# Optimization experiments

Measured on AMD Instinct MI355X. Metric: run time of the kernel, lower is better.

## Reference

```python
import jax, jax.numpy as jnp
import numpy as np

EPS = 1e-5
H_DIM = 64  # hidden_dim


def _bn_relu(x, gamma, beta):
    # torch BatchNorm1d in train mode on [B, C, N]: stats per-channel over (B, N).
    # x here is [B, N, C] (we skip the permutes; math is identical).
    mean = jnp.mean(x, axis=(0, 1))
    var = jnp.var(x, axis=(0, 1))  # biased, matches torch normalization
    return jax.nn.relu((x - mean) * jax.lax.rsqrt(var + EPS) * gamma + beta)


def _make_G(inc):
    # G = DV^{-1/2} H W invDE H^T DV^{-1/2} with W = I, expressed as
    # elementwise diagonal scaling instead of dense diag matmuls.
    H = jax.lax.stop_gradient(inc)  # built under torch.no_grad
    dv = jnp.sum(H, axis=1)  # node degrees [n]
    de = jnp.sum(H, axis=0)  # hyperedge degrees [e]
    Hn = H * (dv ** -0.5)[:, None]          # DV2 @ H
    return (Hn * (1.0 / de)[None, :]) @ Hn.T  # [n, n]


def _gconv_cat(G, node_vec, hidden_flat, W, b, gamma, beta):
    # SHGConv_concate.forward
    B, N, _ = node_vec.shape
    h = hidden_flat.reshape(B, N, H_DIM)
    x = jnp.concatenate([node_vec, h], axis=-1) @ W  # [B, N, out]
    g = jnp.einsum('nm,bmd->bnd', G, x)
    out = _bn_relu(g, gamma, beta) + x + b
    return out.reshape(B, -1)


def _outlayer(G, x0, x1, W0, W1, b, gamma, beta):
    # SHGConv.forward (hidden_dim -> 2)
    h0 = x0 @ W0
    h1 = x1 @ W1
    o0 = _bn_relu(jnp.einsum('nm,bmd->bnd', G, h0), gamma, beta) + h0
    o1 = _bn_relu(jnp.einsum('nm,bmd->bnd', G, h1), gamma, beta) + h1
    return (o0 + o1) / 2.0 + b


def _cell(G, x_t, h, p):
    # STHGCell: GRU-style gating; note torch chunks the FLATTENED [B, N*2H]
    # tensor along dim 1, which we replicate exactly.
    B, N, _ = x_t.shape
    NH = N * H_DIM
    conc = jax.nn.sigmoid(_gconv_cat(G, x_t, h, p['W1'], p['b1'], p['g1'], p['e1']))
    r, u = conc[:, :NH], conc[:, NH:]
    c = jnp.tanh(_gconv_cat(G, x_t, r * h, p['W2'], p['b2'], p['g2'], p['e2']))
    return u * h + (1.0 - u) * c


def setup_inputs() -> dict:
    key = jax.random.key(0)
    ks = jax.random.split(key, 16)
    N, E, D, B, S = 512, 128, 16, 32, 32
    # sparse binary incidence with every node/edge covered (positive degrees)
    Hm = (jax.random.uniform(ks[0], (N, E)) < 0.05).astype(jnp.float32)
    Hm = Hm.at[jnp.arange(N), jnp.arange(N) % E].set(1.0)
    s = 0.1
    return {
        'inputs': jax.random.normal(ks[1], (B, S, N, D), jnp.float32),
        'inc': Hm,
        'gc1_W': jax.random.normal(ks[2], (D + H_DIM, 2 * H_DIM)) * s,
        'gc1_b': jax.random.normal(ks[3], (2 * H_DIM,)) * s,
        'gc1_gamma': jnp.ones((2 * H_DIM,)) + 0.1 * jax.random.normal(ks[4], (2 * H_DIM,)),
        'gc1_beta': jax.random.normal(ks[5], (2 * H_DIM,)) * s,
        'gc2_W': jax.random.normal(ks[6], (D + H_DIM, H_DIM)) * s,
        'gc2_b': jax.random.normal(ks[7], (H_DIM,)) * s,
        'gc2_gamma': jnp.ones((H_DIM,)) + 0.1 * jax.random.normal(ks[8], (H_DIM,)),
        'gc2_beta': jax.random.normal(ks[9], (H_DIM,)) * s,
        'out_W0': jax.random.normal(ks[10], (H_DIM, 2)) * s,
        'out_W1': jax.random.normal(ks[11], (H_DIM, 2)) * s,
        'out_b': jax.random.normal(ks[12], (2,)) * s,
        'out_gamma': jnp.ones((2,)) + 0.1 * jax.random.normal(ks[13], (2,)),
        'out_beta': jax.random.normal(ks[14], (2,)) * s,
    }


def reference(inputs, inc, gc1_W, gc1_b, gc1_gamma, gc1_beta,
              gc2_W, gc2_b, gc2_gamma, gc2_beta,
              out_W0, out_W1, out_b, out_gamma, out_beta):
    B, S, N, D = inputs.shape
    G = _make_G(inc)
    p = dict(W1=gc1_W, b1=gc1_b, g1=gc1_gamma, e1=gc1_beta,
             W2=gc2_W, b2=gc2_b, g2=gc2_gamma, e2=gc2_beta)
    x_tm = jnp.transpose(inputs, (1, 0, 2, 3))  # [S, B, N, D]
    h0 = jnp.zeros((B, N * H_DIM), inputs.dtype)

    def bwd_step(h, xt):
        hn = _cell(G, xt, h, p)
        return hn, hn.reshape(B, N, H_DIM)

    _, feats_b = jax.lax.scan(bwd_step, h0, x_tm[::-1])
    feats1 = feats_b[::-1]  # time order; feats1[t] pairs with forward step t

    def fwd_step(h, xf):
        xt, f1 = xf
        hn = _cell(G, xt, h, p)
        o0 = hn.reshape(B, N, H_DIM)
        pred = _outlayer(G, o0, f1, out_W0, out_W1, out_b, out_gamma, out_beta)
        return hn, (pred, o0)

    _, (preds, feats0) = jax.lax.scan(fwd_step, h0, (x_tm, feats1))
    # 'pred': [B, S, N, 2], 'feat': stacked feats0 [B, S, N, H]
    return jnp.transpose(preds, (1, 0, 2, 3)), jnp.transpose(feats0, (1, 0, 2, 3))
```

## Files before the change

### kernel.cpp

```cpp
#include <hip/hip_runtime.h>
#include <math.h>

#define B_   32
#define S_   32
#define N_   512
#define D_   16
#define H_   64
#define EPS_ 1e-5f
#define CNT_ 16384.0f
#define SNH_ 1048576
#define NH_  32768
#define LDST 72

typedef __attribute__((ext_vector_type(8))) short short8v;
typedef __attribute__((ext_vector_type(8))) _Float16 f16x8;
typedef __attribute__((ext_vector_type(4))) float f32x4;

__device__ __forceinline__ float sigm(float x) { return 1.0f / (1.0f + __expf(-x)); }

__device__ __forceinline__ unsigned short f2h(float x) {
  union { _Float16 h; unsigned short u; } c;
  c.h = (_Float16)x;
  return c.u;
}
__device__ __forceinline__ float h2f(unsigned short u) {
  union { _Float16 h; unsigned short u; } c;
  c.u = u;
  return (float)c.h;
}

__global__ __launch_bounds__(256) void k_deg(const float* __restrict__ Hm,
                                             float* __restrict__ Hs,
                                             float* __restrict__ Hd) {
  __shared__ float sdv[512];
  __shared__ float sde[128];
  __shared__ float tmp[256];
  const int tid = threadIdx.x;
  const int e = tid & 127, half = tid >> 7;
  float p = 0.f;
  for (int r = 0; r < 256; ++r) p += Hm[(half * 256 + r) * 128 + e];
  tmp[tid] = p;
  for (int n = tid; n < 512; n += 256) {
    float s = 0.f;
    for (int k = 0; k < 128; k += 4) {
      float4 v = *(const float4*)&Hm[n * 128 + k];
      s += v.x + v.y + v.z + v.w;
    }
    sdv[n] = s;
  }
  __syncthreads();
  if (tid < 128) sde[tid] = tmp[tid] + tmp[tid + 128];
  __syncthreads();
  for (int i = tid; i < 512 * 128; i += 256) {
    int n = i >> 7, ee = i & 127;
    float hv = Hm[i];
    float hs = hv * rsqrtf(sdv[n]);
    Hs[i] = hs;
    Hd[i] = hs / sde[ee];
  }
}

__global__ __launch_bounds__(256) void g_build(const float* __restrict__ A,
                                               const float* __restrict__ B,
                                               float* __restrict__ C) {
  constexpr int KT = 16;
  __shared__ float As[KT][64];
  __shared__ float Bs[KT][64];
  const int tid = threadIdx.x;
  const int tx = tid & 15, ty = tid >> 4;
  const int n0 = blockIdx.x * 64, m0 = blockIdx.y * 64;
  float acc[4][4];
#pragma unroll
  for (int i = 0; i < 4; ++i)
#pragma unroll
    for (int j = 0; j < 4; ++j) acc[i][j] = 0.f;
  const int ra = tid >> 2, ca = (tid & 3) * 4;
  for (int k0 = 0; k0 < 128; k0 += KT) {
    {
      float4 v = *(const float4*)&A[(size_t)(m0 + ra) * 128 + k0 + ca];
      As[ca + 0][ra] = v.x; As[ca + 1][ra] = v.y;
      As[ca + 2][ra] = v.z; As[ca + 3][ra] = v.w;
    }
    {
      float4 v = *(const float4*)&B[(size_t)(n0 + ra) * 128 + k0 + ca];
      Bs[ca + 0][ra] = v.x; Bs[ca + 1][ra] = v.y;
      Bs[ca + 2][ra] = v.z; Bs[ca + 3][ra] = v.w;
    }
    __syncthreads();
#pragma unroll
    for (int kk = 0; kk < KT; ++kk) {
      float a[4], bv[4];
#pragma unroll
      for (int i = 0; i < 4; ++i) a[i] = As[kk][ty * 4 + i];
#pragma unroll
      for (int j = 0; j < 4; ++j) bv[j] = Bs[kk][tx * 4 + j];
#pragma unroll
      for (int i = 0; i < 4; ++i)
#pragma unroll
        for (int j = 0; j < 4; ++j) acc[i][j] = fmaf(a[i], bv[j], acc[i][j]);
    }
    __syncthreads();
  }
#pragma unroll
  for (int i = 0; i < 4; ++i)
#pragma unroll
    for (int j = 0; j < 4; ++j)
      C[(size_t)(m0 + ty * 4 + i) * 512 + n0 + tx * 4 + j] = acc[i][j];
}

__global__ __launch_bounds__(256) void g2h(const float* __restrict__ G,
                                           unsigned short* __restrict__ Gh) {
  int i = (blockIdx.x * 256 + threadIdx.x) * 4;
  float4 v = *(const float4*)&G[i];
  ushort4 o;
  o.x = f2h(v.x); o.y = f2h(v.y); o.z = f2h(v.z); o.w = f2h(v.w);
  *(ushort4*)&Gh[i] = o;
}

__global__ __launch_bounds__(256) void gmfma(
    const unsigned short* __restrict__ A, const unsigned short* __restrict__ Bf,
    float* __restrict__ C, int Nt, float* __restrict__ stats,
    int chmask, int dirColblks, int dirBase, int sqOff) {
  __shared__ __align__(16) unsigned short As[128 * LDST];
  __shared__ __align__(16) unsigned short Bs[64 * LDST];
  const int tid = threadIdx.x;
  const int lane = tid & 63;
  const int w = tid >> 6, wr = w >> 1, wc = w & 1;
  const int l15 = lane & 15, l4 = lane >> 4;
  const int col0 = blockIdx.x * 64, n0 = blockIdx.y * 128;
  const int srow = tid >> 3, sch = (tid & 7) * 8;

  f32x4 acc[4][2];
#pragma unroll
  for (int mi = 0; mi < 4; ++mi)
#pragma unroll
    for (int ni = 0; ni < 2; ++ni) acc[mi][ni] = (f32x4)0.f;

  short8v pa[4], pb[2];
#pragma unroll
  for (int q = 0; q < 4; ++q)
    pa[q] = *(const short8v*)&A[(size_t)(n0 + srow + q * 32) * 512 + sch];
#pragma unroll
  for (int q = 0; q < 2; ++q)
    pb[q] = *(const short8v*)&Bf[(size_t)(col0 + srow + q * 32) * 512 + sch];

  for (int k0 = 0; k0 < 512; k0 += 64) {
#pragma unroll
    for (int q = 0; q < 4; ++q)
      *(short8v*)&As[(srow + q * 32) * LDST + sch] = pa[q];
#pragma unroll
    for (int q = 0; q < 2; ++q)
      *(short8v*)&Bs[(srow + q * 32) * LDST + sch] = pb[q];
    __syncthreads();
    if (k0 < 448) {
      int kn = k0 + 64;
#pragma unroll
      for (int q = 0; q < 4; ++q)
        pa[q] = *(const short8v*)&A[(size_t)(n0 + srow + q * 32) * 512 + kn + sch];
#pragma unroll
      for (int q = 0; q < 2; ++q)
        pb[q] = *(const short8v*)&Bf[(size_t)(col0 + srow + q * 32) * 512 + kn + sch];
    }
#pragma unroll
    for (int kk = 0; kk < 64; kk += 32) {
      f16x8 av[4], bv[2];
#pragma unroll
      for (int mi = 0; mi < 4; ++mi)
        av[mi] = *(const f16x8*)&As[(wr * 64 + mi * 16 + l15) * LDST + kk + l4 * 8];
#pragma unroll
      for (int ni = 0; ni < 2; ++ni)
        bv[ni] = *(const f16x8*)&Bs[(wc * 32 + ni * 16 + l15) * LDST + kk + l4 * 8];
#pragma unroll
      for (int mi = 0; mi < 4; ++mi)
#pragma unroll
        for (int ni = 0; ni < 2; ++ni)
          acc[mi][ni] = __builtin_amdgcn_mfma_f32_16x16x32_f16(av[mi], bv[ni],
                                                               acc[mi][ni], 0, 0, 0);
    }
    __syncthreads();
  }

  float cs[2] = {0.f, 0.f}, cq[2] = {0.f, 0.f};
#pragma unroll
  for (int mi = 0; mi < 4; ++mi)
#pragma unroll
    for (int ni = 0; ni < 2; ++ni)
#pragma unroll
      for (int r = 0; r < 4; ++r) {
        float val = acc[mi][ni][r];
        C[(size_t)(n0 + wr * 64 + mi * 16 + l4 * 4 + r) * Nt + col0 + wc * 32 + ni * 16 + l15] = val;
        cs[ni] += val;
        cq[ni] = fmaf(val, val, cq[ni]);
      }
  float* red = (float*)As;
  const int owner = wr * 4 + l4;
#pragma unroll
  for (int ni = 0; ni < 2; ++ni) {
    int cb = wc * 32 + ni * 16 + l15;
    red[cb * 8 + owner] = cs[ni];
    red[512 + cb * 8 + owner] = cq[ni];
  }
  __syncthreads();
  if (tid < 64) {
    float s = 0.f, q = 0.f;
    for (int o = 0; o < 8; ++o) { s += red[tid * 8 + o]; q += red[512 + tid * 8 + o]; }
    int base = (blockIdx.x >= dirColblks) ? dirBase : 0;
    int ch = (col0 + tid) & chmask;
    atomicAdd(&stats[base + ch], s);
    atomicAdd(&stats[base + sqOff + ch], q);
  }
}

__global__ __launch_bounds__(512) void prek(
    const float* __restrict__ inp, const float* __restrict__ W1,
    unsigned short* __restrict__ Xf1A, float* __restrict__ h,
    float* __restrict__ st1a, float* __restrict__ stoAll) {
  __shared__ float As[64 * 16];
  __shared__ float Ws[16 * 128];
  const int tid = threadIdx.x, bid = blockIdx.x;
  const int dirb = bid >> 3, m0 = (bid & 7) * 64;
  const int b = dirb & 31;
  const int t0 = (dirb < 32) ? 0 : (S_ - 1);
  float4 z; z.x = 0.f; z.y = 0.f; z.z = 0.f; z.w = 0.f;
  *(float4*)&h[(size_t)dirb * 32768 + m0 * 64 + tid * 8] = z;
  *(float4*)&h[(size_t)dirb * 32768 + m0 * 64 + tid * 8 + 4] = z;
  if (bid == 0) st1a[tid] = 0.f;
  if (bid == 1 && tid < 256) stoAll[tid] = 0.f;
  *(float4*)&Ws[tid * 4] = *(const float4*)&W1[tid * 4];
  {
    int row = tid >> 3, j = tid & 7;
    float2 iv = *(const float2*)&inp[(size_t)((b * S_ + t0) * N_ + m0 + row) * D_ + j * 2];
    As[row * 16 + j * 2] = iv.x;
    As[row * 16 + j * 2 + 1] = iv.y;
  }
  __syncthreads();
  const int tx = tid & 31, ty = tid >> 5;
  float acc[4][4];
#pragma unroll
  for (int i = 0; i < 4; ++i)
#pragma unroll
    for (int j = 0; j < 4; ++j) acc[i][j] = 0.f;
  for (int k = 0; k < 16; ++k) {
    float av[4];
#pragma unroll
    for (int i = 0; i < 4; ++i) av[i] = As[(ty * 4 + i) * 16 + k];
    float4 bv = *(const float4*)&Ws[k * 128 + tx * 4];
    float bva[4] = {bv.x, bv.y, bv.z, bv.w};
#pragma unroll
    for (int i = 0; i < 4; ++i)
#pragma unroll
      for (int j = 0; j < 4; ++j) acc[i][j] = fmaf(av[i], bva[j], acc[i][j]);
  }
#pragma unroll
  for (int j = 0; j < 4; ++j) {
    int g = dirb * 128 + tx * 4 + j;
    ushort4 o;
    o.x = f2h(acc[0][j]); o.y = f2h(acc[1][j]);
    o.z = f2h(acc[2][j]); o.w = f2h(acc[3][j]);
    *(ushort4*)&Xf1A[(size_t)g * 512 + m0 + ty * 4] = o;
  }
}

__global__ __launch_bounds__(512) void cat2k(
    const float* __restrict__ inp, const float* __restrict__ h,
    const float* __restrict__ W2, unsigned short* __restrict__ Xf2,
    const float* __restrict__ G1t, const unsigned short* __restrict__ Xf1C,
    const float* __restrict__ st1c, const float* __restrict__ g1,
    const float* __restrict__ e1, const float* __restrict__ b1,
    float* __restrict__ st2, int tf, int tb) {
  __shared__ float As[80 * 64];
  __shared__ float Ws[80 * 64];
  __shared__ float sm[128], sa[128], sb[128], sbb[128];
  const int tid = threadIdx.x, bid = blockIdx.x;
  const int dirb = bid >> 3, m0 = (bid & 7) * 64;
  const int b = dirb & 31;
  const int dir = (dirb >= 32);
  const int t = dir ? tb : tf;
  if (bid == 0 && tid < 256) st2[tid] = 0.f;
  const float* stp = st1c + (dir ? 256 : 0);
  if (tid < 128) {
    float mean = stp[tid] * (1.f / CNT_);
    float var = fmaf(stp[128 + tid], 1.f / CNT_, -mean * mean);
    float inv = rsqrtf(var + EPS_);
    sm[tid] = mean; sa[tid] = inv * g1[tid];
    sb[tid] = e1[tid]; sbb[tid] = b1[tid];
  }
  for (int i = tid * 4; i < 5120; i += 2048)
    *(float4*)&Ws[i] = *(const float4*)&W2[i];
  __syncthreads();
  const int row = tid >> 3, j = tid & 7;
  const int m = m0 + row;
  if (j < 4) {
    float4 iv = *(const float4*)&inp[(size_t)((b * S_ + t) * N_ + m) * D_ + j * 4];
    As[(j * 4 + 0) * 64 + row] = iv.x; As[(j * 4 + 1) * 64 + row] = iv.y;
    As[(j * 4 + 2) * 64 + row] = iv.z; As[(j * 4 + 3) * 64 + row] = iv.w;
  }
  {
    const int c0 = j * 8;
    const int n = m >> 1;
    const int dd = ((m & 1) << 6) + c0;
    float hva[8], gva[8];
    const float* ph = &h[(size_t)dirb * 32768 + m * 64 + c0];
    const float* pg = &G1t[(size_t)n * 8192 + dirb * 128 + dd];
    *(float4*)&hva[0] = *(const float4*)&ph[0];
    *(float4*)&hva[4] = *(const float4*)&ph[4];
    *(float4*)&gva[0] = *(const float4*)&pg[0];
    *(float4*)&gva[4] = *(const float4*)&pg[4];
#pragma unroll
    for (int i = 0; i < 8; ++i) {
      int d2 = dd + i;
      float x1v = h2f(Xf1C[(size_t)(dirb * 128 + d2) * 512 + n]);
      float pre = fmaf(gva[i] - sm[d2], sa[d2], sb[d2]);
      pre = fmaxf(pre, 0.f) + x1v + sbb[d2];
      As[(16 + c0 + i) * 64 + row] = sigm(pre) * hva[i];
    }
  }
  __syncthreads();
  const int tx = tid & 15, ty = tid >> 4;
  float acc[2][4];
#pragma unroll
  for (int i = 0; i < 2; ++i)
#pragma unroll
    for (int jj = 0; jj < 4; ++jj) acc[i][jj] = 0.f;
  for (int k = 0; k < 80; ++k) {
    float a0 = As[k * 64 + ty * 2], a1 = As[k * 64 + ty * 2 + 1];
    float4 bv = *(const float4*)&Ws[k * 64 + tx * 4];
    float bva[4] = {bv.x, bv.y, bv.z, bv.w};
#pragma unroll
    for (int jj = 0; jj < 4; ++jj) {
      acc[0][jj] = fmaf(a0, bva[jj], acc[0][jj]);
      acc[1][jj] = fmaf(a1, bva[jj], acc[1][jj]);
    }
  }
#pragma unroll
  for (int jj = 0; jj < 4; ++jj) {
    int g = dirb * 64 + tx * 4 + jj;
    ushort2 o;
    o.x = f2h(acc[0][jj]); o.y = f2h(acc[1][jj]);
    *(ushort2*)&Xf2[(size_t)g * 512 + m0 + ty * 2] = o;
  }
}

__global__ __launch_bounds__(512) void eltk(
    const float* __restrict__ inp, const float* __restrict__ G1t,
    const unsigned short* __restrict__ Xf1C, const float* __restrict__ st1c,
    const float* __restrict__ g1, const float* __restrict__ e1,
    const float* __restrict__ b1, const float* __restrict__ G2t,
    const unsigned short* __restrict__ Xf2, const float* __restrict__ st2,
    const float* __restrict__ g2, const float* __restrict__ e2,
    const float* __restrict__ b2, float* __restrict__ h,
    float* __restrict__ out1, const float* __restrict__ W1,
    unsigned short* __restrict__ Xf1N, const float* __restrict__ W0o,
    const float* __restrict__ W1o, unsigned short* __restrict__ Xo16,
    int tf, int tb, int doX1, float* __restrict__ stn) {
  __shared__ float As[64 * 80];
  __shared__ float Ws[80 * 128];
  __shared__ float sW0[128], sW1[128];
  const int tid = threadIdx.x, bid = blockIdx.x;
  const int dirb = bid >> 3, m0 = (bid & 7) * 64;
  const int b = dirb & 31;
  const int dir = (dirb >= 32);
  const int t = dir ? tb : tf;
  const int nextT = dir ? (tb - 1) : (tf + 1);
  if (bid == 0) stn[tid] = 0.f;
  if (tid < 128) { sW0[tid] = W0o[tid]; sW1[tid] = W1o[tid]; }
  __syncthreads();

  const int row = tid >> 3, co = (tid & 7) * 8;
  const int m = m0 + row;
  const int mh = m >> 1;
  const int du0 = ((m & 1) << 6) + co;
  const float* stp = st1c + (dir ? 256 : 0);
  const float* st2p = st2 + (dir ? 128 : 0);
  float g1a[8], g2a[8], ha[8];
  {
    const float* p1 = &G1t[(size_t)(256 + mh) * 8192 + dirb * 128 + du0];
    const float* p3 = &G2t[(size_t)m * 4096 + dirb * 64 + co];
    const float* p5 = &h[(size_t)dirb * 32768 + m * 64 + co];
    *(float4*)&g1a[0] = *(const float4*)&p1[0];
    *(float4*)&g1a[4] = *(const float4*)&p1[4];
    *(float4*)&g2a[0] = *(const float4*)&p3[0];
    *(float4*)&g2a[4] = *(const float4*)&p3[4];
    *(float4*)&ha[0] = *(const float4*)&p5[0];
    *(float4*)&ha[4] = *(const float4*)&p5[4];
  }
  float hn[8];
#pragma unroll
  for (int i = 0; i < 8; ++i) {
    int du = du0 + i;
    float x1v = h2f(Xf1C[(size_t)(dirb * 128 + du) * 512 + 256 + mh]);
    float mean = stp[du] * (1.f / CNT_);
    float var = stp[128 + du] * (1.f / CNT_) - mean * mean;
    float inv = rsqrtf(var + EPS_);
    float pre = fmaxf((g1a[i] - mean) * inv * g1[du] + e1[du], 0.f) + x1v + b1[du];
    float u = sigm(pre);
    int dc = co + i;
    float x2v = h2f(Xf2[(size_t)(dirb * 64 + dc) * 512 + m]);
    float mean2 = st2p[dc] * (1.f / CNT_);
    float var2 = st2p[64 + dc] * (1.f / CNT_) - mean2 * mean2;
    float inv2 = rsqrtf(var2 + EPS_);
    float pre2 = fmaxf((g2a[i] - mean2) * inv2 * g2[dc] + e2[dc], 0.f) + x2v + b2[dc];
    float cc = tanhf(pre2);
    hn[i] = u * ha[i] + (1.f - u) * cc;
  }
  {
    float* ph = &h[(size_t)dirb * 32768 + m * 64 + co];
    *(float4*)&ph[0] = *(const float4*)&hn[0];
    *(float4*)&ph[4] = *(const float4*)&hn[4];
  }
  *(float4*)&As[row * 80 + 16 + co] = *(const float4*)&hn[0];
  *(float4*)&As[row * 80 + 16 + co + 4] = *(const float4*)&hn[4];
  if (!dir) {
    float* po = &out1[(size_t)b * SNH_ + (size_t)t * NH_ + m * 64 + co];
    *(float4*)&po[0] = *(const float4*)&hn[0];
    *(float4*)&po[4] = *(const float4*)&hn[4];
  }
  {
    const float* sW = dir ? sW1 : sW0;
    float p0 = 0.f, p1 = 0.f;
#pragma unroll
    for (int jj = 0; jj < 8; ++jj) {
      int c = co + jj;
      p0 = fmaf(hn[jj], sW[c * 2], p0);
      p1 = fmaf(hn[jj], sW[c * 2 + 1], p1);
    }
#pragma unroll
    for (int off = 1; off < 8; off <<= 1) {
      p0 += __shfl_xor(p0, off);
      p1 += __shfl_xor(p1, off);
    }
    if ((tid & 7) == 0) {
      int colb = (dir ? 2048 : 0) + b * 64 + t * 2;
      Xo16[(size_t)colb * 512 + m] = f2h(p0);
      Xo16[(size_t)(colb + 1) * 512 + m] = f2h(p1);
    }
  }

  if (doX1) {
    {
      int ri = tid >> 3, k2 = (tid & 7) * 2;
      float2 iv = *(const float2*)&inp[(size_t)((b * S_ + nextT) * N_ + m0 + ri) * D_ + k2];
      As[ri * 80 + k2] = iv.x;
      As[ri * 80 + k2 + 1] = iv.y;
    }
    for (int i = tid * 4; i < 10240; i += 2048)
      *(float4*)&Ws[i] = *(const float4*)&W1[i];
    __syncthreads();
    const int tx = tid & 31, ty = tid >> 5;
    float acc[4][4];
#pragma unroll
    for (int i = 0; i < 4; ++i)
#pragma unroll
      for (int jj = 0; jj < 4; ++jj) acc[i][jj] = 0.f;
    for (int k = 0; k < 80; ++k) {
      float av[4];
#pragma unroll
      for (int i = 0; i < 4; ++i) av[i] = As[(ty * 4 + i) * 80 + k];
      float4 bv = *(const float4*)&Ws[k * 128 + tx * 4];
      float bva[4] = {bv.x, bv.y, bv.z, bv.w};
#pragma unroll
      for (int i = 0; i < 4; ++i)
#pragma unroll
        for (int jj = 0; jj < 4; ++jj) acc[i][jj] = fmaf(av[i], bva[jj], acc[i][jj]);
    }
#pragma unroll
    for (int jj = 0; jj < 4; ++jj) {
      int g = dirb * 128 + tx * 4 + jj;
      ushort4 o;
      o.x = f2h(acc[0][jj]); o.y = f2h(acc[1][jj]);
      o.z = f2h(acc[2][jj]); o.w = f2h(acc[3][jj]);
      *(ushort4*)&Xf1N[(size_t)g * 512 + m0 + ty * 4] = o;
    }
  }
}

__global__ __launch_bounds__(512) void outfinalk(
    const float* __restrict__ Got, const unsigned short* __restrict__ Xo16,
    const float* __restrict__ sto, const float* __restrict__ go,
    const float* __restrict__ eo, const float* __restrict__ bo,
    float* __restrict__ out0) {
  __shared__ float sst[256];
  const int tid = threadIdx.x;
  if (tid < 256) sst[tid] = sto[tid];
  __syncthreads();
  const int pos = (blockIdx.x * 512 + tid) * 4;
  const int b = pos >> 14, r = pos & 16383;
  const int t = r >> 9, n0 = r & 511;
  const int colb = b * 64 + t * 2;
  float outv[8];
#pragma unroll
  for (int p = 0; p < 2; ++p) {
    int ch0 = t * 2 + p, ch1 = 64 + t * 2 + p;
    float mean0 = sst[ch0] * (1.f / CNT_);
    float var0 = sst[128 + ch0] * (1.f / CNT_) - mean0 * mean0;
    float inv0 = rsqrtf(var0 + EPS_) * go[p];
    float mean1 = sst[ch1] * (1.f / CNT_);
    float var1 = sst[128 + ch1] * (1.f / CNT_) - mean1 * mean1;
    float inv1 = rsqrtf(var1 + EPS_) * go[p];
#pragma unroll
    for (int k = 0; k < 4; ++k) {
      float got0 = Got[(size_t)(n0 + k) * 4096 + colb + p];
      float got1 = Got[(size_t)(n0 + k) * 4096 + 2048 + colb + p];
      float h0 = h2f(Xo16[(size_t)(colb + p) * 512 + n0 + k]);
      float h1 = h2f(Xo16[(size_t)(2048 + colb + p) * 512 + n0 + k]);
      float o0 = fmaxf((got0 - mean0) * inv0 + eo[p], 0.f) + h0;
      float o1 = fmaxf((got1 - mean1) * inv1 + eo[p], 0.f) + h1;
      outv[k * 2 + p] = 0.5f * (o0 + o1) + bo[p];
    }
  }
  float4 v0; v0.x = outv[0]; v0.y = outv[1]; v0.z = outv[2]; v0.w = outv[3];
  float4 v1; v1.x = outv[4]; v1.y = outv[5]; v1.z = outv[6]; v1.w = outv[7];
  *(float4*)&out0[(size_t)pos * 2] = v0;
  *(float4*)&out0[(size_t)pos * 2 + 4] = v1;
}

extern "C" void kernel_launch(void* const* d_in, const int* in_sizes, int n_in,
                              void* d_out, int out_size, void* d_ws, size_t ws_size,
                              hipStream_t stream) {
  (void)in_sizes; (void)n_in; (void)out_size; (void)ws_size;
  const float* inp = (const float*)d_in[0];
  const float* inc = (const float*)d_in[1];
  const float* W1 = (const float*)d_in[2];
  const float* b1 = (const float*)d_in[3];
  const float* g1 = (const float*)d_in[4];
  const float* e1 = (const float*)d_in[5];
  const float* W2 = (const float*)d_in[6];
  const float* b2 = (const float*)d_in[7];
  const float* g2 = (const float*)d_in[8];
  const float* e2 = (const float*)d_in[9];
  const float* W0o = (const float*)d_in[10];
  const float* W1o = (const float*)d_in[11];
  const float* bo = (const float*)d_in[12];
  const float* go = (const float*)d_in[13];
  const float* eo = (const float*)d_in[14];

  float* ws = (float*)d_ws;
  float* G    = ws;
  float* Hs   = G + 262144;
  float* Hd   = Hs + 65536;
  float* h    = Hd + 65536;
  float* G1t  = h + 2097152;
  float* G2t  = G1t + 4194304;
  float* st1a = G2t + 2097152;
  float* st1b = st1a + 512;
  float* st2  = st1b + 512;
  float* sto  = st2 + 256;
  float* after = st1a + 2048;
  unsigned short* Gh   = (unsigned short*)after;
  unsigned short* Xf1A = (unsigned short*)(after + 131072);
  unsigned short* Xf1B = (unsigned short*)(after + 131072 + 2097152);
  unsigned short* Xf2  = (unsigned short*)(after + 131072 + 2 * 2097152);
  unsigned short* Xo16 = (unsigned short*)(after + 131072 + 2 * 2097152 + 1048576);

  float* out0 = (float*)d_out;
  float* out1 = out0 + (size_t)B_ * S_ * N_ * 2;

  k_deg<<<1, 256, 0, stream>>>(inc, Hs, Hd);
  g_build<<<dim3(8, 8), 256, 0, stream>>>(Hd, Hs, G);
  g2h<<<256, 256, 0, stream>>>(G, Gh);
  prek<<<512, 512, 0, stream>>>(inp, W1, Xf1A, h, st1a, sto);

  for (int ti = 0; ti < S_; ++ti) {
    const int tf = ti, tb = S_ - 1 - ti;
    float* stc = (ti & 1) ? st1b : st1a;
    float* stn = (ti & 1) ? st1a : st1b;
    unsigned short* xf1C = (ti & 1) ? Xf1B : Xf1A;
    unsigned short* xf1N = (ti & 1) ? Xf1A : Xf1B;
    const int doX1 = (ti < S_ - 1) ? 1 : 0;

    gmfma<<<dim3(128, 4), 256, 0, stream>>>(Gh, xf1C, G1t, 8192, stc,
                                            127, 64, 256, 128);
    cat2k<<<512, 512, 0, stream>>>(inp, h, W2, Xf2, G1t, xf1C, stc, g1, e1, b1,
                                   st2, tf, tb);
    gmfma<<<dim3(64, 4), 256, 0, stream>>>(Gh, Xf2, G2t, 4096, st2,
                                           63, 32, 128, 64);
    eltk<<<512, 512, 0, stream>>>(inp, G1t, xf1C, stc, g1, e1, b1, G2t, Xf2,
                                  st2, g2, e2, b2, h, out1, W1, xf1N, W0o, W1o,
                                  Xo16, tf, tb, doX1, stn);
  }

  gmfma<<<dim3(64, 4), 256, 0, stream>>>(Gh, Xo16, G1t, 4096, sto,
                                         63, 32, 64, 128);
  outfinalk<<<256, 512, 0, stream>>>(G1t, Xo16, sto, go, eo, bo, out0);
}
```

Baseline: 2.737 ms.

## Store graph-conv outputs in fp16 and add row-major activation copies for gathers

The MFMA graph-convolution kernel now writes its output tiles as fp16 instead of fp32, which halves the intermediate traffic read back by cat2k, eltk and outfinalk. The producer kernels also write a second, row-major fp16 copy of the linear-projection outputs (Xr1/Xr2). This lets the elementwise kernels read 8 contiguous half values per load instead of gathering scalar halves with a 512-element stride. Xf1 becomes a single buffer, since only the next step's MFMA reads it. The cost is extra write bandwidth for the duplicate layouts and reduced precision in the stored G@x results; the BatchNorm statistics are still accumulated from fp32.

```diff
diff --git a/kernel.cpp b/kernel.cpp
--- a/kernel.cpp
+++ b/kernel.cpp
@@ -27,6 +27,11 @@
   union { _Float16 h; unsigned short u; } c;
   c.u = u;
   return (float)c.h;
+}
+__device__ __forceinline__ void ld8h(const unsigned short* p, float* o) {
+  f16x8 v = *(const f16x8*)p;
+#pragma unroll
+  for (int i = 0; i < 8; ++i) o[i] = (float)v[i];
 }
 
 __global__ __launch_bounds__(256) void k_deg(const float* __restrict__ Hm,
@@ -119,7 +124,7 @@
 
 __global__ __launch_bounds__(256) void gmfma(
     const unsigned short* __restrict__ A, const unsigned short* __restrict__ Bf,
-    float* __restrict__ C, int Nt, float* __restrict__ stats,
+    unsigned short* __restrict__ C, int Nt, float* __restrict__ stats,
     int chmask, int dirColblks, int dirBase, int sqOff) {
   __shared__ __align__(16) unsigned short As[128 * LDST];
   __shared__ __align__(16) unsigned short Bs[64 * LDST];
@@ -188,7 +193,7 @@
 #pragma unroll
       for (int r = 0; r < 4; ++r) {
         float val = acc[mi][ni][r];
-        C[(size_t)(n0 + wr * 64 + mi * 16 + l4 * 4 + r) * Nt + col0 + wc * 32 + ni * 16 + l15] = val;
+        C[(size_t)(n0 + wr * 64 + mi * 16 + l4 * 4 + r) * Nt + col0 + wc * 32 + ni * 16 + l15] = f2h(val);
         cs[ni] += val;
         cq[ni] = fmaf(val, val, cq[ni]);
       }
@@ -213,8 +218,8 @@
 
 __global__ __launch_bounds__(512) void prek(
     const float* __restrict__ inp, const float* __restrict__ W1,
-    unsigned short* __restrict__ Xf1A, float* __restrict__ h,
-    float* __restrict__ st1a, float* __restrict__ stoAll) {
+    unsigned short* __restrict__ Xf1, unsigned short* __restrict__ Xr1A,
+    float* __restrict__ h, float* __restrict__ st1a, float* __restrict__ sto) {
   __shared__ float As[64 * 16];
   __shared__ float Ws[16 * 128];
   const int tid = threadIdx.x, bid = blockIdx.x;
@@ -225,7 +230,7 @@
   *(float4*)&h[(size_t)dirb * 32768 + m0 * 64 + tid * 8] = z;
   *(float4*)&h[(size_t)dirb * 32768 + m0 * 64 + tid * 8 + 4] = z;
   if (bid == 0) st1a[tid] = 0.f;
-  if (bid == 1 && tid < 256) stoAll[tid] = 0.f;
+  if (bid == 1 && tid < 256) sto[tid] = 0.f;
   *(float4*)&Ws[tid * 4] = *(const float4*)&W1[tid * 4];
   {
     int row = tid >> 3, j = tid & 7;
@@ -257,14 +262,22 @@
     ushort4 o;
     o.x = f2h(acc[0][j]); o.y = f2h(acc[1][j]);
     o.z = f2h(acc[2][j]); o.w = f2h(acc[3][j]);
-    *(ushort4*)&Xf1A[(size_t)g * 512 + m0 + ty * 4] = o;
+    *(ushort4*)&Xf1[(size_t)g * 512 + m0 + ty * 4] = o;
+  }
+#pragma unroll
+  for (int i = 0; i < 4; ++i) {
+    ushort4 o;
+    o.x = f2h(acc[i][0]); o.y = f2h(acc[i][1]);
+    o.z = f2h(acc[i][2]); o.w = f2h(acc[i][3]);
+    *(ushort4*)&Xr1A[((size_t)dirb * 512 + m0 + ty * 4 + i) * 128 + tx * 4] = o;
   }
 }
 
 __global__ __launch_bounds__(512) void cat2k(
     const float* __restrict__ inp, const float* __restrict__ h,
     const float* __restrict__ W2, unsigned short* __restrict__ Xf2,
-    const float* __restrict__ G1t, const unsigned short* __restrict__ Xf1C,
+    unsigned short* __restrict__ Xr2,
+    const unsigned short* __restrict__ G1h, const unsigned short* __restrict__ Xr1C,
     const float* __restrict__ st1c, const float* __restrict__ g1,
     const float* __restrict__ e1, const float* __restrict__ b1,
     float* __restrict__ st2, int tf, int tb) {
@@ -299,19 +312,17 @@
     const int c0 = j * 8;
     const int n = m >> 1;
     const int dd = ((m & 1) << 6) + c0;
-    float hva[8], gva[8];
+    float hva[8], gva[8], xva[8];
     const float* ph = &h[(size_t)dirb * 32768 + m * 64 + c0];
-    const float* pg = &G1t[(size_t)n * 8192 + dirb * 128 + dd];
     *(float4*)&hva[0] = *(const float4*)&ph[0];
     *(float4*)&hva[4] = *(const float4*)&ph[4];
-    *(float4*)&gva[0] = *(const float4*)&pg[0];
-    *(float4*)&gva[4] = *(const float4*)&pg[4];
+    ld8h(&G1h[(size_t)n * 8192 + dirb * 128 + dd], gva);
+    ld8h(&Xr1C[((size_t)dirb * 512 + n) * 128 + dd], xva);
 #pragma unroll
     for (int i = 0; i < 8; ++i) {
       int d2 = dd + i;
-      float x1v = h2f(Xf1C[(size_t)(dirb * 128 + d2) * 512 + n]);
       float pre = fmaf(gva[i] - sm[d2], sa[d2], sb[d2]);
-      pre = fmaxf(pre, 0.f) + x1v + sbb[d2];
+      pre = fmaxf(pre, 0.f) + xva[i] + sbb[d2];
       As[(16 + c0 + i) * 64 + row] = sigm(pre) * hva[i];
     }
   }
@@ -339,19 +350,27 @@
     o.x = f2h(acc[0][jj]); o.y = f2h(acc[1][jj]);
     *(ushort2*)&Xf2[(size_t)g * 512 + m0 + ty * 2] = o;
   }
+#pragma unroll
+  for (int i = 0; i < 2; ++i) {
+    ushort4 o;
+    o.x = f2h(acc[i][0]); o.y = f2h(acc[i][1]);
+    o.z = f2h(acc[i][2]); o.w = f2h(acc[i][3]);
+    *(ushort4*)&Xr2[((size_t)dirb * 512 + m0 + ty * 2 + i) * 64 + tx * 4] = o;
+  }
 }
 
 __global__ __launch_bounds__(512) void eltk(
-    const float* __restrict__ inp, const float* __restrict__ G1t,
-    const unsigned short* __restrict__ Xf1C, const float* __restrict__ st1c,
+    const float* __restrict__ inp, const unsigned short* __restrict__ G1h,
+    const unsigned short* __restrict__ Xr1C, const float* __restrict__ st1c,
     const float* __restrict__ g1, const float* __restrict__ e1,
-    const float* __restrict__ b1, const float* __restrict__ G2t,
-    const unsigned short* __restrict__ Xf2, const float* __restrict__ st2,
+    const float* __restrict__ b1, const unsigned short* __restrict__ G2h,
+    const unsigned short* __restrict__ Xr2, const float* __restrict__ st2,
     const float* __restrict__ g2, const float* __restrict__ e2,
     const float* __restrict__ b2, float* __restrict__ h,
     float* __restrict__ out1, const float* __restrict__ W1,
-    unsigned short* __restrict__ Xf1N, const float* __restrict__ W0o,
-    const float* __restrict__ W1o, unsigned short* __restrict__ Xo16,
+    unsigned short* __restrict__ Xf1, unsigned short* __restrict__ Xr1N,
+    const float* __restrict__ W0o, const float* __restrict__ W1o,
+    unsigned short* __restrict__ Xo16,
     int tf, int tb, int doX1, float* __restrict__ stn) {
   __shared__ float As[64 * 80];
   __shared__ float Ws[80 * 128];
@@ -372,34 +391,30 @@
   const int du0 = ((m & 1) << 6) + co;
   const float* stp = st1c + (dir ? 256 : 0);
   const float* st2p = st2 + (dir ? 128 : 0);
-  float g1a[8], g2a[8], ha[8];
+  float g1a[8], g2a[8], ha[8], x1a[8], x2a[8];
   {
-    const float* p1 = &G1t[(size_t)(256 + mh) * 8192 + dirb * 128 + du0];
-    const float* p3 = &G2t[(size_t)m * 4096 + dirb * 64 + co];
     const float* p5 = &h[(size_t)dirb * 32768 + m * 64 + co];
-    *(float4*)&g1a[0] = *(const float4*)&p1[0];
-    *(float4*)&g1a[4] = *(const float4*)&p1[4];
-    *(float4*)&g2a[0] = *(const float4*)&p3[0];
-    *(float4*)&g2a[4] = *(const float4*)&p3[4];
     *(float4*)&ha[0] = *(const float4*)&p5[0];
     *(float4*)&ha[4] = *(const float4*)&p5[4];
+    ld8h(&G1h[(size_t)(256 + mh) * 8192 + dirb * 128 + du0], g1a);
+    ld8h(&G2h[(size_t)m * 4096 + dirb * 64 + co], g2a);
+    ld8h(&Xr1C[((size_t)dirb * 512 + 256 + mh) * 128 + du0], x1a);
+    ld8h(&Xr2[((size_t)dirb * 512 + m) * 64 + co], x2a);
   }
   float hn[8];
 #pragma unroll
   for (int i = 0; i < 8; ++i) {
     int du = du0 + i;
-    float x1v = h2f(Xf1C[(size_t)(dirb * 128 + du) * 512 + 256 + mh]);
     float mean = stp[du] * (1.f / CNT_);
     float var = stp[128 + du] * (1.f / CNT_) - mean * mean;
     float inv = rsqrtf(var + EPS_);
-    float pre = fmaxf((g1a[i] - mean) * inv * g1[du] + e1[du], 0.f) + x1v + b1[du];
+    float pre = fmaxf((g1a[i] - mean) * inv * g1[du] + e1[du], 0.f) + x1a[i] + b1[du];
     float u = sigm(pre);
     int dc = co + i;
-    float x2v = h2f(Xf2[(size_t)(dirb * 64 + dc) * 512 + m]);
     float mean2 = st2p[dc] * (1.f / CNT_);
     float var2 = st2p[64 + dc] * (1.f / CNT_) - mean2 * mean2;
     float inv2 = rsqrtf(var2 + EPS_);
-    float pre2 = fmaxf((g2a[i] - mean2) * inv2 * g2[dc] + e2[dc], 0.f) + x2v + b2[dc];
+    float pre2 = fmaxf((g2a[i] - mean2) * inv2 * g2[dc] + e2[dc], 0.f) + x2a[i] + b2[dc];
     float cc = tanhf(pre2);
     hn[i] = u * ha[i] + (1.f - u) * cc;
   }
@@ -469,13 +484,20 @@
       ushort4 o;
       o.x = f2h(acc[0][jj]); o.y = f2h(acc[1][jj]);
       o.z = f2h(acc[2][jj]); o.w = f2h(acc[3][jj]);
-      *(ushort4*)&Xf1N[(size_t)g * 512 + m0 + ty * 4] = o;
+      *(ushort4*)&Xf1[(size_t)g * 512 + m0 + ty * 4] = o;
+    }
+#pragma unroll
+    for (int i = 0; i < 4; ++i) {
+      ushort4 o;
+      o.x = f2h(acc[i][0]); o.y = f2h(acc[i][1]);
+      o.z = f2h(acc[i][2]); o.w = f2h(acc[i][3]);
+      *(ushort4*)&Xr1N[((size_t)dirb * 512 + m0 + ty * 4 + i) * 128 + tx * 4] = o;
     }
   }
 }
 
 __global__ __launch_bounds__(512) void outfinalk(
-    const float* __restrict__ Got, const unsigned short* __restrict__ Xo16,
+    const unsigned short* __restrict__ Got, const unsigned short* __restrict__ Xo16,
     const float* __restrict__ sto, const float* __restrict__ go,
     const float* __restrict__ eo, const float* __restrict__ bo,
     float* __restrict__ out0) {
@@ -499,8 +521,8 @@
     float inv1 = rsqrtf(var1 + EPS_) * go[p];
 #pragma unroll
     for (int k = 0; k < 4; ++k) {
-      float got0 = Got[(size_t)(n0 + k) * 4096 + colb + p];
-      float got1 = Got[(size_t)(n0 + k) * 4096 + 2048 + colb + p];
+      float got0 = h2f(Got[(size_t)(n0 + k) * 4096 + colb + p]);
+      float got1 = h2f(Got[(size_t)(n0 + k) * 4096 + 2048 + colb + p]);
       float h0 = h2f(Xo16[(size_t)(colb + p) * 512 + n0 + k]);
       float h1 = h2f(Xo16[(size_t)(2048 + colb + p) * 512 + n0 + k]);
       float o0 = fmaxf((got0 - mean0) * inv0 + eo[p], 0.f) + h0;
@@ -539,18 +561,20 @@
   float* Hs   = G + 262144;
   float* Hd   = Hs + 65536;
   float* h    = Hd + 65536;
-  float* G1t  = h + 2097152;
-  float* G2t  = G1t + 4194304;
-  float* st1a = G2t + 2097152;
+  float* st1a = h + 2097152;
   float* st1b = st1a + 512;
   float* st2  = st1b + 512;
   float* sto  = st2 + 256;
   float* after = st1a + 2048;
   unsigned short* Gh   = (unsigned short*)after;
-  unsigned short* Xf1A = (unsigned short*)(after + 131072);
-  unsigned short* Xf1B = (unsigned short*)(after + 131072 + 2097152);
-  unsigned short* Xf2  = (unsigned short*)(after + 131072 + 2 * 2097152);
-  unsigned short* Xo16 = (unsigned short*)(after + 131072 + 2 * 2097152 + 1048576);
+  unsigned short* G1h  = Gh + 262144;
+  unsigned short* G2h  = G1h + 4194304;
+  unsigned short* Xf1  = G2h + 2097152;
+  unsigned short* Xr1A = Xf1 + 4194304;
+  unsigned short* Xr1B = Xr1A + 4194304;
+  unsigned short* Xf2  = Xr1B + 4194304;
+  unsigned short* Xr2  = Xf2 + 2097152;
+  unsigned short* Xo16 = Xr2 + 2097152;
 
   float* out0 = (float*)d_out;
   float* out1 = out0 + (size_t)B_ * S_ * N_ * 2;
@@ -558,28 +582,28 @@
   k_deg<<<1, 256, 0, stream>>>(inc, Hs, Hd);
   g_build<<<dim3(8, 8), 256, 0, stream>>>(Hd, Hs, G);
   g2h<<<256, 256, 0, stream>>>(G, Gh);
-  prek<<<512, 512, 0, stream>>>(inp, W1, Xf1A, h, st1a, sto);
+  prek<<<512, 512, 0, stream>>>(inp, W1, Xf1, Xr1A, h, st1a, sto);
 
   for (int ti = 0; ti < S_; ++ti) {
     const int tf = ti, tb = S_ - 1 - ti;
     float* stc = (ti & 1) ? st1b : st1a;
     float* stn = (ti & 1) ? st1a : st1b;
-    unsigned short* xf1C = (ti & 1) ? Xf1B : Xf1A;
-    unsigned short* xf1N = (ti & 1) ? Xf1A : Xf1B;
+    unsigned short* xr1C = (ti & 1) ? Xr1B : Xr1A;
+    unsigned short* xr1N = (ti & 1) ? Xr1A : Xr1B;
     const int doX1 = (ti < S_ - 1) ? 1 : 0;
 
-    gmfma<<<dim3(128, 4), 256, 0, stream>>>(Gh, xf1C, G1t, 8192, stc,
+    gmfma<<<dim3(128, 4), 256, 0, stream>>>(Gh, Xf1, G1h, 8192, stc,
                                             127, 64, 256, 128);
-    cat2k<<<512, 512, 0, stream>>>(inp, h, W2, Xf2, G1t, xf1C, stc, g1, e1, b1,
-                                   st2, tf, tb);
-    gmfma<<<dim3(64, 4), 256, 0, stream>>>(Gh, Xf2, G2t, 4096, st2,
+    cat2k<<<512, 512, 0, stream>>>(inp, h, W2, Xf2, Xr2, G1h, xr1C, stc,
+                                   g1, e1, b1, st2, tf, tb);
+    gmfma<<<dim3(64, 4), 256, 0, stream>>>(Gh, Xf2, G2h, 4096, st2,
                                            63, 32, 128, 64);
-    eltk<<<512, 512, 0, stream>>>(inp, G1t, xf1C, stc, g1, e1, b1, G2t, Xf2,
-                                  st2, g2, e2, b2, h, out1, W1, xf1N, W0o, W1o,
-                                  Xo16, tf, tb, doX1, stn);
-  }
-
-  gmfma<<<dim3(64, 4), 256, 0, stream>>>(Gh, Xo16, G1t, 4096, sto,
+    eltk<<<512, 512, 0, stream>>>(inp, G1h, xr1C, stc, g1, e1, b1, G2h, Xr2,
+                                  st2, g2, e2, b2, h, out1, W1, Xf1, xr1N,
+                                  W0o, W1o, Xo16, tf, tb, doX1, stn);
+  }
+
+  gmfma<<<dim3(64, 4), 256, 0, stream>>>(Gh, Xo16, G1h, 4096, sto,
                                          63, 32, 64, 128);
-  outfinalk<<<256, 512, 0, stream>>>(G1t, Xo16, sto, go, eo, bo, out0);
-}
+  outfinalk<<<256, 512, 0, stream>>>(G1h, Xo16, sto, go, eo, bo, out0);
+}
```

New measurement: 2.488 ms. 1.1x faster.
